# Performance work log

Hardware: AMD Instinct MI355X
Metric: run time of the kernel (lower is better)

## Reference

```python
import jax, jax.numpy as jnp
import numpy as np

M1, M2, BS = 2000, 400, 8
AT = M1 + M2
E1, E2, E3 = 60000, 20000, 20000
H, F, NG, L, C = 64, 64, 50, 4, 4
CUTOFF = 10.0
LOG2 = 0.6931471805599453  # shift of ShiftedSoftplus


def _ssp(x):
    return jax.nn.softplus(x) - LOG2


def _smear(d):
    # GaussianSmearing(0, cutoff, NG)
    offset = jnp.linspace(0.0, CUTOFF, NG)
    coeff = -0.5 / (offset[1] - offset[0]) ** 2
    return jnp.exp(coeff * (d[:, None] - offset[None, :]) ** 2)  # [E, NG]


def _colored_mlp(attr, colors, w1, b1, w2, b2):
    # w1:[C,NG,F] b1:[C,F] w2:[C,F,F] b2:[C,F]; route each edge through its color's MLP
    out = jnp.zeros((attr.shape[0], w1.shape[-1]), attr.dtype)
    for c in range(C):  # fixed small color count
        h = _ssp(attr @ w1[c] + b1[c]) @ w2[c] + b2[c]
        out = out + jnp.where((colors == c)[:, None], h, jnp.zeros((), attr.dtype))
    return out


def _block(h, ei, ew, attr, col, p):
    # InteractionBlock: CFConv -> ssp -> linear
    mw1, mb1, mw2, mb2, cw1, cw2, cb2, bw, bb = p
    Ccut = 0.5 * (jnp.cos(ew * jnp.pi / CUTOFF) + 1.0)
    W = _colored_mlp(attr, col, mw1, mb1, mw2, mb2) * Ccut[:, None]  # [E,F]
    x = h @ cw1                                   # lin1 (no bias) [N,F]
    msg = x[ei[:, 0]] * W                         # gather x_j, modulate
    agg = jax.ops.segment_sum(msg, ei[:, 1], num_segments=h.shape[0])  # scatter-add
    x = agg @ cw2 + cb2                           # lin2
    return _ssp(x) @ bw + bb                      # act + block linear


def _batch_graph(ei, ew, col):
    # replicate per-structure edges across the batch with node offset b*AT
    offs = (jnp.arange(BS, dtype=ei.dtype) * AT)[:, None, None]
    ei_b = (ei[None] + offs).reshape(-1, 2)
    return ei_b, jnp.tile(ew, BS), jnp.tile(col, BS)


def _forward(sites, sites_p, e1, ew1, c1, e2, ew2, c2, e3, ew3, c3,
             emb_w, emb_p_w, mlp_w1, mlp_b1, mlp_w2, mlp_b2,
             conv_w1, conv_w2, conv_b2, blk_w, blk_b,
             out_w1, out_b1, out_w2, out_b2):
    h = jnp.concatenate([emb_w[sites], emb_p_w[sites_p]], axis=1).reshape(BS * AT, H)
    graphs = []
    for (ei, ew, col) in ((e1, ew1, c1), (e2, ew2, c2), (e3, ew3, c3)):
        ei_b, ew_b, col_b = _batch_graph(ei, ew, col)
        graphs.append((ei_b, ew_b, col_b, _smear(ew_b)))
    for l in range(L):
        delta = jnp.zeros_like(h)
        for g, (ei_b, ew_b, col_b, attr_b) in enumerate(graphs):
            p = (mlp_w1[l, g], mlp_b1[l, g], mlp_w2[l, g], mlp_b2[l, g],
                 conv_w1[l, g], conv_w2[l, g], conv_b2[l, g], blk_w[l, g], blk_b[l, g])
            delta = delta + _block(h, ei_b, ew_b, attr_b, col_b, p)
        h = h + delta
    hp = h.reshape(BS, AT, H)[:, M1:, :]   # mask selects pore nodes only
    o = hp @ out_w1 + out_b1               # NB: original has `h - self.act(h)` no-op, so no activation here
    o = o @ out_w2 + out_b2                # [BS, M2, 1]
    return o.sum(axis=1)                   # 'add' readout per batch -> [BS, 1]


def setup_inputs() -> dict:
    key = jax.random.key(0)
    ks = jax.random.split(key, 24)
    f = lambda i, shape, s=0.1: jax.random.normal(ks[i], shape, jnp.float32) * s
    sites = jax.random.randint(ks[0], (BS, M1), 0, 1, dtype=jnp.int32)
    sites_p = jax.random.randint(ks[1], (BS, M2), 0, 2, dtype=jnp.int32)
    e1 = jax.random.randint(ks[2], (E1, 2), 0, M1, dtype=jnp.int32)
    e2 = jnp.stack([jax.random.randint(ks[3], (E2,), 0, M1, dtype=jnp.int32),
                    jax.random.randint(ks[4], (E2,), M1, AT, dtype=jnp.int32)], 1)
    e3 = jnp.stack([jax.random.randint(ks[5], (E3,), M1, AT, dtype=jnp.int32),
                    jax.random.randint(ks[6], (E3,), 0, M1, dtype=jnp.int32)], 1)
    ew1 = jax.random.uniform(ks[7], (E1,), jnp.float32, 0.5, CUTOFF)
    ew2 = jax.random.uniform(ks[8], (E2,), jnp.float32, 0.5, CUTOFF)
    ew3 = jax.random.uniform(ks[9], (E3,), jnp.float32, 0.5, CUTOFF)
    c1 = jax.random.randint(ks[10], (E1,), 0, C, dtype=jnp.int32)
    c2 = jax.random.randint(ks[11], (E2,), 0, C, dtype=jnp.int32)
    c3 = jax.random.randint(ks[12], (E3,), 0, C, dtype=jnp.int32)
    return {
        'sites': sites, 'sites_p': sites_p,
        'edge_idx1': e1, 'edge_weight1': ew1, 'colors1': c1,
        'edge_idx2': e2, 'edge_weight2': ew2, 'colors2': c2,
        'edge_idx3': e3, 'edge_weight3': ew3, 'colors3': c3,
        'emb_w': f(13, (1, H), 1.0), 'emb_p_w': f(14, (2, H), 1.0),
        'mlp_w1': f(15, (L, 3, C, NG, F)), 'mlp_b1': jnp.zeros((L, 3, C, F), jnp.float32),
        'mlp_w2': f(16, (L, 3, C, F, F)), 'mlp_b2': jnp.zeros((L, 3, C, F), jnp.float32),
        'conv_w1': f(17, (L, 3, H, F)), 'conv_w2': f(18, (L, 3, F, H)),
        'conv_b2': jnp.zeros((L, 3, H), jnp.float32),
        'blk_w': f(19, (L, 3, H, H)), 'blk_b': jnp.zeros((L, 3, H), jnp.float32),
        'out_w1': f(20, (H, H // 2)), 'out_b1': jnp.zeros((H // 2,), jnp.float32),
        'out_w2': f(21, (H // 2, 1)), 'out_b2': jnp.zeros((1,), jnp.float32),
    }


def reference(sites, sites_p, edge_idx1, edge_weight1, colors1,
              edge_idx2, edge_weight2, colors2, edge_idx3, edge_weight3, colors3,
              emb_w, emb_p_w, mlp_w1, mlp_b1, mlp_w2, mlp_b2,
              conv_w1, conv_w2, conv_b2, blk_w, blk_b,
              out_w1, out_b1, out_w2, out_b2):
    return _forward(sites, sites_p, edge_idx1, edge_weight1, colors1,
                    edge_idx2, edge_weight2, colors2, edge_idx3, edge_weight3, colors3,
                    emb_w, emb_p_w, mlp_w1, mlp_b1, mlp_w2, mlp_b2,
                    conv_w1, conv_w2, conv_b2, blk_w, blk_b,
                    out_w1, out_b1, out_w2, out_b2)
```

## Files before the change

### kernel.cpp

```cpp
#include <hip/hip_runtime.h>
#include <math.h>

constexpr int M1 = 2000, M2 = 400, BS = 8;
constexpr int AT = M1 + M2;
constexpr int NN = BS * AT;
constexpr int E1 = 60000, E2 = 20000, E3 = 20000;
constexpr int ET = E1 + E2 + E3;
constexpr int H = 64, F = 64, NG = 50, L = 4, C = 4;
constexpr float CUTOFF = 10.0f;
constexpr float LOG2F_ = 0.6931471805599453f;

constexpr float SMEAR_STEP = 10.0f / 49.0f;
constexpr float SMEAR_COEFF = -12.005f;
constexpr float PI_OVER_CUT = 0.31415926535897932f;

constexpr int NBLK = (ET + 255) / 256;

constexpr int NT = 256;
constexpr float DSCALE = (float)(NT - 1) / CUTOFF;

constexpr int GP0 = E1 + 3 * M1;
constexpr int GP1 = E2 + 3 * M2;
constexpr int GP2 = E3 + 3 * M1;
constexpr int ETP = GP0 + GP1 + GP2;

constexpr int TILE_M = 32;

constexpr int SITE_T = M1 / 4;
constexpr int PORE_T = M2 / 4;
constexpr int NBLK_L = 2 * (SITE_T + PORE_T);

constexpr int LT0 = M1 / 4;
constexpr int LT1 = M1 / 4;
constexpr int LT2 = M2 / 4;
constexpr int LTOT = LT0 + LT1 + LT2;
constexpr int PADB = (3 * AT + 255) / 256;

constexpr int A_TAB  = 192;
constexpr int A_INIT = NN * 64 / 256;
constexpr int A_CNT  = NBLK;
constexpr int A_CV   = 3;
constexpr int A_TOT  = A_TAB + A_INIT + A_CNT + A_CV;
constexpr int B_PACK = 48 * NT * 64 / 256;
constexpr int B_TOT  = B_PACK + 3 + 2;

constexpr size_t O_HA    = 0;
constexpr size_t O_HB    = O_HA  + (size_t)NN * 64 * 4;
constexpr size_t O_XG    = O_HB  + (size_t)NN * 64 * 4;
constexpr size_t O_TABF  = O_XG  + (size_t)3 * 2 * AT * 256 * 4;
constexpr size_t O_TAB2  = O_TABF + (size_t)48 * NT * 64 * 4;
constexpr size_t O_EDATA = O_TAB2 + (size_t)48 * NT * 64 * 4;
constexpr size_t O_INT   = O_EDATA + (size_t)ETP * 16;
constexpr int I_DEG  = 0;
constexpr int I_CUR  = 7200;
constexpr int I_ZEND = 14400;
constexpr int I_BASE = 14400;
constexpr int I_PERM = 21616;
constexpr int I_CV   = 26016;

__device__ inline float sspf(float x) {
    return fmaxf(x, 0.0f) + log1pf(expf(-fabsf(x))) - LOG2F_;
}
__device__ inline float sspf_fast(float x) {
    float t = __expf(-fabsf(x));
    return fmaxf(x, 0.0f) + __logf(1.0f + t) - LOG2F_;
}

__device__ inline unsigned int bf16rn(float x) {
    unsigned int u = __float_as_uint(x);
    u = (u + 0x7FFFu + ((u >> 16) & 1u)) >> 16;
    return u & 0xFFFFu;
}

__device__ inline int graph_off(int g) { return g == 0 ? 0 : (g == 1 ? GP0 : GP0 + GP1); }

__device__ inline void edge_decode(int idx, int& g, int& e,
                                   const int* ei1, const int* ei2, const int* ei3,
                                   const int* c1, const int* c2, const int* c3,
                                   const int*& ei, const int*& cl) {
    if (idx < E1)            { g = 0; e = idx;           ei = ei1; cl = c1; }
    else if (idx < E1 + E2)  { g = 1; e = idx - E1;      ei = ei2; cl = c2; }
    else                     { g = 2; e = idx - E1 - E2; ei = ei3; cl = c3; }
}

__global__ __launch_bounds__(256) void k_setupA(
    const float* __restrict__ mlp_w1, const float* __restrict__ mlp_b1,
    const float* __restrict__ mlp_w2, const float* __restrict__ mlp_b2,
    float* __restrict__ tabF,
    const int* __restrict__ sites, const int* __restrict__ sites_p,
    const float* __restrict__ emb_w, const float* __restrict__ emb_p_w,
    float* __restrict__ h,
    const int* __restrict__ ei1, const int* __restrict__ ei2,
    const int* __restrict__ ei3, const int* __restrict__ c1,
    const int* __restrict__ c2, const int* __restrict__ c3,
    int* __restrict__ deg,
    const float* __restrict__ conv_b2, const float* __restrict__ blk_w,
    const float* __restrict__ blk_b, float* __restrict__ cvbuf) {
    int bid = blockIdx.x;
    int t = threadIdx.x;
    if (bid < A_TAB) {
        const int lane = t & 63;
        int wslot = bid * 4 + (t >> 6);
        int s = wslot >> 4;
        int pq = wslot & 15;
        int l = s % L;
        int gc = s / L;
        int c = gc % C;
        int g = gc / C;
        size_t wb = (size_t)((l * 3 + g) * C + c);
        const float* w1 = mlp_w1 + wb * NG * F;
        const float* w2 = mlp_w2 + wb * F * F;
        float w1c[NG], w2c[F];
        #pragma unroll
        for (int k = 0; k < NG; k++) w1c[k] = w1[k * F + lane];
        #pragma unroll
        for (int k = 0; k < F; k++) w2c[k] = w2[k * F + lane];
        float b1c = mlp_b1[wb * F + lane];
        float b2c = mlp_b2[wb * F + lane];
        for (int pp = 0; pp < 16; pp++) {
            int p = pq * 16 + pp;
            float d = (float)p * (CUTOFF / (float)(NT - 1));
            float dd = d - (float)lane * SMEAR_STEP;
            float av = (lane < NG) ? __expf(SMEAR_COEFF * dd * dd) : 0.0f;
            float acc = b1c;
            #pragma unroll
            for (int k = 0; k < NG; k++) acc = fmaf(__shfl(av, k), w1c[k], acc);
            float tt = sspf_fast(acc);
            float acc2 = b2c;
            #pragma unroll
            for (int j = 0; j < F; j++) acc2 = fmaf(__shfl(tt, j), w2c[j], acc2);
            float ccut = 0.5f * (__cosf(d * PI_OVER_CUT) + 1.0f);
            tabF[((size_t)s * NT + p) * 64 + lane] = acc2 * ccut;
        }
    } else if (bid < A_TAB + A_INIT) {
        int idx = (bid - A_TAB) * 256 + t;
        int f = idx & 63;
        int n = idx >> 6;
        int b = n / AT;
        int i = n - b * AT;
        float v;
        if (i < M1) v = emb_w[sites[b * M1 + i] * H + f];
        else        v = emb_p_w[sites_p[b * M2 + (i - M1)] * H + f];
        h[idx] = v;
    } else if (bid < A_TAB + A_INIT + A_CNT) {
        int idx = (bid - A_TAB - A_INIT) * 256 + t;
        if (idx < ET) {
            int g, e; const int* ei; const int* cl;
            edge_decode(idx, g, e, ei1, ei2, ei3, c1, c2, c3, ei, cl);
            atomicAdd(&deg[g * AT + ei[2 * e + 1]], 1);
        }
    } else {
        int s = (bid - A_TAB - A_INIT - A_CNT) * 4 + (t >> 6);
        int lane = t & 63;
        if (s < 12) {
            float sl = sspf(conv_b2[s * 64 + lane]);
            const float* bw = blk_w + (size_t)s * 4096;
            float a = blk_b[s * 64 + lane];
            #pragma unroll 8
            for (int k = 0; k < 64; k++)
                a = fmaf(__shfl(sl, k), bw[k * 64 + lane], a);
            cvbuf[s * 64 + lane] = a;
        }
    }
}

__global__ __launch_bounds__(256) void k_setupB(
    const float* __restrict__ tabF, unsigned int* __restrict__ tab2,
    const int* __restrict__ deg, int* __restrict__ base,
    int* __restrict__ perm) {
    int bid = blockIdx.x;
    int t = threadIdx.x;
    if (bid < B_PACK) {
        int idx = bid * 256 + t;
        int pc = idx & (NT * 64 - 1);
        int nxt = (pc < (NT - 1) * 64) ? idx + 64 : idx;
        unsigned int lo = bf16rn(tabF[idx]);
        unsigned int hi = bf16rn(tabF[nxt]);
        tab2[idx] = lo | (hi << 16);
    } else if (bid < B_PACK + 3) {
        const int T = 256, CH = 10;
        __shared__ int lsum[256];
        int g = bid - B_PACK;
        int loc[CH];
        int s = 0;
        #pragma unroll
        for (int i = 0; i < CH; i++) {
            int idx = t * CH + i;
            int v = (idx < AT) ? ((deg[g * AT + idx] + 3) & ~3) : 0;
            loc[i] = s;
            s += v;
        }
        lsum[t] = s;
        __syncthreads();
        for (int off = 1; off < T; off <<= 1) {
            int v = 0;
            if (t >= off) v = lsum[t - off];
            __syncthreads();
            lsum[t] += v;
            __syncthreads();
        }
        int tb = lsum[t] - s;
        #pragma unroll
        for (int i = 0; i < CH; i++) {
            int idx = t * CH + i;
            if (idx < AT) base[g * (AT + 1) + idx] = tb + loc[i];
        }
        if (t == T - 1) base[g * (AT + 1) + AT] = lsum[T - 1];
    } else {
        __shared__ int hist[256];
        __shared__ int cur[256];
        int q = bid - B_PACK - 3;
        int cnt   = q ? M2 : M1;
        int obase = q ? M1 : 0;
        hist[t] = 0;
        __syncthreads();
        for (int i = t; i < cnt; i += 256) {
            int key = q ? deg[AT + M1 + i] : (deg[i] + deg[2 * AT + i]);
            atomicAdd(&hist[min(key, 255)], 1);
        }
        __syncthreads();
        if (t == 0) {
            int run = 0;
            for (int k = 0; k < 256; k++) { cur[k] = run; run += hist[k]; }
        }
        __syncthreads();
        for (int i = t; i < cnt; i += 256) {
            int key = q ? deg[AT + M1 + i] : (deg[i] + deg[2 * AT + i]);
            int pos = atomicAdd(&cur[min(key, 255)], 1);
            perm[obase + pos] = q ? (M1 + i) : i;
        }
    }
}

__device__ inline void fma4(float acc[4], float a, const float4 b) {
    acc[0] = fmaf(a, b.x, acc[0]);
    acc[1] = fmaf(a, b.y, acc[1]);
    acc[2] = fmaf(a, b.z, acc[2]);
    acc[3] = fmaf(a, b.w, acc[3]);
}

__device__ inline void stage_B(const float* __restrict__ gB, float (*Bs)[68], int t) {
    #pragma unroll
    for (int i = 0; i < 4; i++) {
        int v = t + i * 256;
        int r = v >> 4, c4 = (v & 15) * 4;
        *(float4*)&Bs[r][c4] = *(const float4*)(gB + (size_t)r * 64 + c4);
    }
}
struct WReg { float4 v0, v1, v2, v3; };
__device__ inline WReg stage_ld(const float* __restrict__ g, int t) {
    int r0 = t >> 4, c4 = (t & 15) * 4;
    WReg w;
    w.v0 = *(const float4*)(g + (size_t)r0 * 64 + c4);
    w.v1 = *(const float4*)(g + (size_t)(r0 + 16) * 64 + c4);
    w.v2 = *(const float4*)(g + (size_t)(r0 + 32) * 64 + c4);
    w.v3 = *(const float4*)(g + (size_t)(r0 + 48) * 64 + c4);
    return w;
}
__device__ inline void stage_st(const WReg& w, float (*Bs)[68], int t) {
    int r0 = t >> 4, c4 = (t & 15) * 4;
    *(float4*)&Bs[r0][c4]      = w.v0;
    *(float4*)&Bs[r0 + 16][c4] = w.v1;
    *(float4*)&Bs[r0 + 32][c4] = w.v2;
    *(float4*)&Bs[r0 + 48][c4] = w.v3;
}

__device__ inline void gemm_tile(const float (*As)[68], const float (*Bs)[68],
                                 int r0, int c0, float acc0[4], float acc1[4]) {
    #pragma unroll 4
    for (int k0 = 0; k0 < 64; k0 += 4) {
        float4 a0 = *(const float4*)&As[r0][k0];
        float4 a1 = *(const float4*)&As[r0 + 1][k0];
        float4 b0 = *(const float4*)&Bs[k0][c0];
        float4 b1 = *(const float4*)&Bs[k0 + 1][c0];
        float4 b2 = *(const float4*)&Bs[k0 + 2][c0];
        float4 b3 = *(const float4*)&Bs[k0 + 3][c0];
        fma4(acc0, a0.x, b0); fma4(acc0, a0.y, b1);
        fma4(acc0, a0.z, b2); fma4(acc0, a0.w, b3);
        fma4(acc1, a1.x, b0); fma4(acc1, a1.y, b1);
        fma4(acc1, a1.z, b2); fma4(acc1, a1.w, b3);
    }
}
__device__ inline void gemm_row(const float (*As)[68], const float (*Bs)[68],
                                int r, int c0, float acc[4]) {
    #pragma unroll 4
    for (int k0 = 0; k0 < 64; k0 += 4) {
        float4 a = *(const float4*)&As[r][k0];
        float4 b0 = *(const float4*)&Bs[k0][c0];
        float4 b1 = *(const float4*)&Bs[k0 + 1][c0];
        float4 b2 = *(const float4*)&Bs[k0 + 2][c0];
        float4 b3 = *(const float4*)&Bs[k0 + 3][c0];
        fma4(acc, a.x, b0); fma4(acc, a.y, b1);
        fma4(acc, a.z, b2); fma4(acc, a.w, b3);
    }
}

__device__ inline void xg_store8(const float (*T)[68], float* __restrict__ xg,
                                 int g, int i0, int t) {
    int k = t >> 6, c = t & 63;
    float* o0 = xg + (((size_t)(g * 2 + 0) * AT + i0 + k) * 64 + c) * 4;
    float* o1 = xg + (((size_t)(g * 2 + 1) * AT + i0 + k) * 64 + c) * 4;
    *(float4*)o0 = make_float4(T[k * 8 + 0][c], T[k * 8 + 1][c],
                               T[k * 8 + 2][c], T[k * 8 + 3][c]);
    *(float4*)o1 = make_float4(T[k * 8 + 4][c], T[k * 8 + 5][c],
                               T[k * 8 + 6][c], T[k * 8 + 7][c]);
}
__device__ inline void xg_store4(const float (*T)[68], float* __restrict__ xg,
                                 int g, int bh, const int* __restrict__ perm,
                                 int pbase, int gi, int t) {
    int k = t >> 6, c = t & 63;
    int node = perm[pbase + gi * 4 + k];
    float* out = xg + (((size_t)(g * 2 + bh) * AT + node) * 64 + c) * 4;
    *(float4*)out = make_float4(T[k * 4 + 0][c], T[k * 4 + 1][c],
                                T[k * 4 + 2][c], T[k * 4 + 3][c]);
}

__device__ inline float tab_lerp(unsigned int u, int z) {
    float lo = __uint_as_float(u << 16);
    float hi = __uint_as_float(u & 0xFFFF0000u);
    return fmaf(__int_as_float(z), hi - lo, lo);
}

__device__ inline void gather4(const int4* __restrict__ ed, int s, int e,
                               const unsigned int* __restrict__ tg,
                               const float* __restrict__ xgg,
                               int lane, float acc[4]) {
    for (int i = s; i < e; i += 4) {
        int4 e0 = ed[i];
        int4 e1 = ed[i + 1];
        int4 e2 = ed[i + 2];
        int4 e3 = ed[i + 3];
        unsigned int u0 = tg[(size_t)e0.y * 64 + lane];
        unsigned int u1 = tg[(size_t)e1.y * 64 + lane];
        unsigned int u2 = tg[(size_t)e2.y * 64 + lane];
        unsigned int u3 = tg[(size_t)e3.y * 64 + lane];
        float4 q0 = *(const float4*)(xgg + ((size_t)e0.x << 8) + lane * 4);
        float4 q1 = *(const float4*)(xgg + ((size_t)e1.x << 8) + lane * 4);
        float4 q2 = *(const float4*)(xgg + ((size_t)e2.x << 8) + lane * 4);
        float4 q3 = *(const float4*)(xgg + ((size_t)e3.x << 8) + lane * 4);
        float wl0 = tab_lerp(u0, e0.z);
        float wl1 = tab_lerp(u1, e1.z);
        float wl2 = tab_lerp(u2, e2.z);
        float wl3 = tab_lerp(u3, e3.z);
        fma4(acc, wl0, q0);
        fma4(acc, wl1, q1);
        fma4(acc, wl2, q2);
        fma4(acc, wl3, q3);
    }
}

__global__ __launch_bounds__(256) void k_layer(
    const int4* __restrict__ edata, const int* __restrict__ base,
    const int* __restrict__ perm,
    float* __restrict__ xg, const unsigned int* __restrict__ tab2,
    const float* __restrict__ conv_w2, const float* __restrict__ conv_b2,
    const float* __restrict__ blk_w, const float* __restrict__ blk_b,
    const float* __restrict__ conv_w1, const float* __restrict__ cvbuf,
    const float* __restrict__ hIn, float* __restrict__ hOut,
    int l, int last) {
    __shared__ float As[16][68];
    __shared__ float Ps[16][68];
    __shared__ float Bs[64][68];
    const int t = threadIdx.x;
    const int lane = t & 63;
    const int wv = t >> 6;
    int bid = blockIdx.x;
    int site, tile, bh;
    if (bid < 2 * SITE_T) { site = 1; tile = bid >> 1; bh = bid & 1; }
    else { site = 0; tile = (bid - 2 * SITE_T) >> 1; bh = (bid - 2 * SITE_T) & 1; }
    const int gi = site ? (SITE_T - 1 - tile) : (PORE_T - 1 - tile);
    const int pbperm = site ? 0 : M1;
    const int gA = site ? 0 : 1;
    const size_t pbA = (size_t)(l * 3 + gA);
    const size_t pbB = (size_t)(l * 3 + 2);

    WReg R = stage_ld(conv_w2 + pbA * 4096, t);

    const int dst = __builtin_amdgcn_readfirstlane(perm[pbperm + gi * 4 + wv]);
    float accA[4] = {0, 0, 0, 0}, accB[4] = {0, 0, 0, 0};
    {
        int s = __builtin_amdgcn_readfirstlane(base[gA * (AT + 1) + dst]);
        int e = __builtin_amdgcn_readfirstlane(base[gA * (AT + 1) + dst + 1]);
        gather4(edata + graph_off(gA), s, e,
                tab2 + ((size_t)gA * C * L + l) * NT * 64,
                xg + (size_t)(gA * 2 + bh) * AT * 256, lane, accA);
    }
    if (site) {
        int s = __builtin_amdgcn_readfirstlane(base[2 * (AT + 1) + dst]);
        int e = __builtin_amdgcn_readfirstlane(base[2 * (AT + 1) + dst + 1]);
        gather4(edata + graph_off(2), s, e,
                tab2 + ((size_t)2 * C * L + l) * NT * 64,
                xg + (size_t)(2 * 2 + bh) * AT * 256, lane, accB);
    }
    #pragma unroll
    for (int b = 0; b < 4; b++) As[wv * 4 + b][lane] = accA[b];
    stage_st(R, Bs, t);
    R = stage_ld(blk_w + pbA * 4096, t);
    __syncthreads();

    const int r = t >> 4;
    const int c0 = (t & 15) * 4;
    const int k = r >> 2, bl = r & 3;
    const int node = perm[pbperm + gi * 4 + k];
    const int batch = bh * 4 + bl;
    const size_t o = ((size_t)batch * AT + node) * 64 + c0;
    const float* cvl = cvbuf + (size_t)l * 3 * 64;

    float4 cb = *(const float4*)(conv_b2 + pbA * 64 + c0);
    float x[4] = {cb.x, cb.y, cb.z, cb.w};
    gemm_row(As, Bs, r, c0, x);
    __syncthreads();
    *(float4*)&As[r][c0] =
        make_float4(sspf(x[0]), sspf(x[1]), sspf(x[2]), sspf(x[3]));
    stage_st(R, Bs, t);
    if (site) R = stage_ld(conv_w2 + pbB * 4096, t);
    else if (!last) R = stage_ld(conv_w1 + (size_t)((l + 1) * 3 + 2) * 4096, t);
    __syncthreads();

    float4 hv = *(const float4*)(hIn + o);
    float4 bbA = *(const float4*)(blk_b + pbA * 64 + c0);
    float d[4];
    if (site) {
        float4 bbB = *(const float4*)(blk_b + pbB * 64 + c0);
        float4 cv1 = *(const float4*)(cvl + 64 + c0);
        d[0] = hv.x + bbA.x + bbB.x + cv1.x;
        d[1] = hv.y + bbA.y + bbB.y + cv1.y;
        d[2] = hv.z + bbA.z + bbB.z + cv1.z;
        d[3] = hv.w + bbA.w + bbB.w + cv1.w;
    } else {
        float4 cv0 = *(const float4*)(cvl + c0);
        float4 cv2 = *(const float4*)(cvl + 128 + c0);
        d[0] = hv.x + bbA.x + cv0.x + cv2.x;
        d[1] = hv.y + bbA.y + cv0.y + cv2.y;
        d[2] = hv.z + bbA.z + cv0.z + cv2.z;
        d[3] = hv.w + bbA.w + cv0.w + cv2.w;
    }
    gemm_row(As, Bs, r, c0, d);
    if (site) {
        __syncthreads();
        #pragma unroll
        for (int b = 0; b < 4; b++) As[wv * 4 + b][lane] = accB[b];
        stage_st(R, Bs, t);
        R = stage_ld(blk_w + pbB * 4096, t);
        __syncthreads();
        float4 cb2v = *(const float4*)(conv_b2 + pbB * 64 + c0);
        float y[4] = {cb2v.x, cb2v.y, cb2v.z, cb2v.w};
        gemm_row(As, Bs, r, c0, y);
        __syncthreads();
        *(float4*)&As[r][c0] =
            make_float4(sspf(y[0]), sspf(y[1]), sspf(y[2]), sspf(y[3]));
        stage_st(R, Bs, t);
        if (!last) R = stage_ld(conv_w1 + (size_t)((l + 1) * 3 + 0) * 4096, t);
        __syncthreads();
        gemm_row(As, Bs, r, c0, d);
    }
    *(float4*)(hOut + o) = make_float4(d[0], d[1], d[2], d[3]);
    if (last) return;

    __syncthreads();
    *(float4*)&As[r][c0] = make_float4(d[0], d[1], d[2], d[3]);
    stage_st(R, Bs, t);
    if (site) R = stage_ld(conv_w1 + (size_t)((l + 1) * 3 + 1) * 4096, t);
    __syncthreads();
    float p[4] = {0, 0, 0, 0};
    gemm_row(As, Bs, r, c0, p);
    __syncthreads();
    *(float4*)&Ps[r][c0] = make_float4(p[0], p[1], p[2], p[3]);
    if (site) stage_st(R, Bs, t);
    __syncthreads();
    xg_store4(Ps, xg, site ? 0 : 2, bh, perm, pbperm, gi, t);
    if (site) {
        float q[4] = {0, 0, 0, 0};
        gemm_row(As, Bs, r, c0, q);
        __syncthreads();
        *(float4*)&Ps[r][c0] = make_float4(q[0], q[1], q[2], q[3]);
        __syncthreads();
        xg_store4(Ps, xg, 1, bh, perm, pbperm, gi, t);
    }
}

__global__ __launch_bounds__(256) void k_fl(
    const int* __restrict__ ei1, const int* __restrict__ ei2,
    const int* __restrict__ ei3, const int* __restrict__ c1,
    const int* __restrict__ c2, const int* __restrict__ c3,
    const float* __restrict__ ew1, const float* __restrict__ ew2,
    const float* __restrict__ ew3,
    const int* __restrict__ base, int* __restrict__ cur,
    const int* __restrict__ deg, int4* __restrict__ edata,
    const float* __restrict__ h, const float* __restrict__ conv_w1,
    float* __restrict__ xg) {
    __shared__ float As[TILE_M][68];
    __shared__ float Bs[64][68];
    int t = threadIdx.x;
    if (blockIdx.x >= LTOT + NBLK) {
        int idx = (blockIdx.x - LTOT - NBLK) * 256 + t;
        if (idx >= 3 * AT) return;
        int g = idx / AT, dn = idx - g * AT;
        int d = deg[g * AT + dn];
        int pd = (d + 3) & ~3;
        int4* ep = edata + graph_off(g) + base[g * (AT + 1) + dn] + d;
        for (int k2 = 0; k2 < pd - d; k2++) ep[k2] = make_int4(0, NT - 1, 0, 0);
        return;
    }
    if (blockIdx.x >= LTOT) {
        int idx = (blockIdx.x - LTOT) * 256 + t;
        if (idx >= ET) return;
        int g, e; const int* ei; const int* cl;
        edge_decode(idx, g, e, ei1, ei2, ei3, c1, c2, c3, ei, cl);
        const float* ew = (g == 0) ? ew1 : (g == 1 ? ew2 : ew3);
        int dst = ei[2 * e + 1];
        int src = ei[2 * e];
        int p = base[g * (AT + 1) + dst] + atomicAdd(&cur[g * AT + dst], 1);
        float tt = ew[e] * DSCALE;
        int i0 = min((int)tt, NT - 2);
        float fr = tt - (float)i0;
        int cb = cl[e] * (L * NT) + i0;
        edata[graph_off(g) + p] = make_int4(src, cb, __float_as_int(fr), 0);
        return;
    }
    int g, igrp;
    {
        int bid = blockIdx.x;
        if (bid < LT0)            { g = 0; igrp = bid; }
        else if (bid < LT0 + LT1) { g = 1; igrp = bid - LT0; }
        else                      { g = 2; igrp = LT0 + (bid - LT0 - LT1); }
    }
    int i0 = igrp * 4;
    #pragma unroll
    for (int it = 0; it < 2; it++) {
        int v = t + it * 256;
        int r = v >> 4, c4 = (v & 15) * 4;
        int n = (r & 7) * AT + i0 + (r >> 3);
        *(float4*)&As[r][c4] = *(const float4*)(h + (size_t)n * 64 + c4);
    }
    stage_B(conv_w1 + (size_t)g * 4096, Bs, t);
    __syncthreads();
    int cg = t & 15, rg = t >> 4;
    int c0 = cg * 4, r0 = rg * 2;
    float acc0[4] = {0, 0, 0, 0}, acc1[4] = {0, 0, 0, 0};
    gemm_tile(As, Bs, r0, c0, acc0, acc1);
    __syncthreads();
    *(float4*)&As[r0][c0]     = make_float4(acc0[0], acc0[1], acc0[2], acc0[3]);
    *(float4*)&As[r0 + 1][c0] = make_float4(acc1[0], acc1[1], acc1[2], acc1[3]);
    __syncthreads();
    xg_store8(As, xg, g, i0, t);
}

__global__ void k_read(const float* __restrict__ h,
                       const float* __restrict__ w1, const float* __restrict__ b1,
                       const float* __restrict__ w2, const float* __restrict__ b2,
                       float* __restrict__ out) {
    int b = blockIdx.x;
    int lane = threadIdx.x & 63;
    int wv = threadIdx.x >> 6;
    __shared__ float part[4];
    float weff = 0.0f;
    #pragma unroll
    for (int j = 0; j < H / 2; j++) weff = fmaf(w1[lane * (H / 2) + j], w2[j], weff);
    float acc = 0.0f;
    for (int i = wv * (M2 / 4); i < (wv + 1) * (M2 / 4); i++)
        acc += h[((size_t)b * AT + M1 + i) * H + lane];
    float v = acc * weff;
    for (int off = 32; off; off >>= 1) v += __shfl_xor(v, off);
    if (lane == 0) part[wv] = v;
    __syncthreads();
    if (threadIdx.x == 0) {
        float bias = b2[0];
        for (int j = 0; j < H / 2; j++) bias = fmaf(b1[j], w2[j], bias);
        out[b] = part[0] + part[1] + part[2] + part[3] + (float)M2 * bias;
    }
}

extern "C" void kernel_launch(void* const* d_in, const int* in_sizes, int n_in,
                              void* d_out, int out_size, void* d_ws, size_t ws_size,
                              hipStream_t stream) {
    const int* sites   = (const int*)d_in[0];
    const int* sites_p = (const int*)d_in[1];
    const int* ei1 = (const int*)d_in[2];
    const float* ew1 = (const float*)d_in[3];
    const int* c1 = (const int*)d_in[4];
    const int* ei2 = (const int*)d_in[5];
    const float* ew2 = (const float*)d_in[6];
    const int* c2 = (const int*)d_in[7];
    const int* ei3 = (const int*)d_in[8];
    const float* ew3 = (const float*)d_in[9];
    const int* c3 = (const int*)d_in[10];
    const float* emb_w   = (const float*)d_in[11];
    const float* emb_p_w = (const float*)d_in[12];
    const float* mlp_w1 = (const float*)d_in[13];
    const float* mlp_b1 = (const float*)d_in[14];
    const float* mlp_w2 = (const float*)d_in[15];
    const float* mlp_b2 = (const float*)d_in[16];
    const float* conv_w1 = (const float*)d_in[17];
    const float* conv_w2 = (const float*)d_in[18];
    const float* conv_b2 = (const float*)d_in[19];
    const float* blk_w = (const float*)d_in[20];
    const float* blk_b = (const float*)d_in[21];
    const float* out_w1 = (const float*)d_in[22];
    const float* out_b1 = (const float*)d_in[23];
    const float* out_w2 = (const float*)d_in[24];
    const float* out_b2 = (const float*)d_in[25];

    char* ws = (char*)d_ws;
    float* hA   = (float*)(ws + O_HA);
    float* hB   = (float*)(ws + O_HB);
    float* xg   = (float*)(ws + O_XG);
    float* tabF = (float*)(ws + O_TABF);
    unsigned int* tab2 = (unsigned int*)(ws + O_TAB2);
    int4*  edata = (int4*)(ws + O_EDATA);
    int* ip    = (int*)(ws + O_INT);
    int* deg   = ip + I_DEG;
    int* cur   = ip + I_CUR;
    int* ibase = ip + I_BASE;
    int* dperm = ip + I_PERM;
    float* cvbuf = (float*)(ip + I_CV);

    hipMemsetAsync(ip, 0, (size_t)I_ZEND * sizeof(int), stream);

    k_setupA<<<A_TOT, 256, 0, stream>>>(mlp_w1, mlp_b1, mlp_w2, mlp_b2, tabF,
                                        sites, sites_p, emb_w, emb_p_w, hA,
                                        ei1, ei2, ei3, c1, c2, c3, deg,
                                        conv_b2, blk_w, blk_b, cvbuf);
    k_setupB<<<B_TOT, 256, 0, stream>>>(tabF, tab2, deg, ibase, dperm);
    k_fl<<<LTOT + NBLK + PADB, 256, 0, stream>>>(ei1, ei2, ei3, c1, c2, c3,
                                                 ew1, ew2, ew3, ibase, cur, deg,
                                                 edata, hA, conv_w1, xg);

    float* hcur = hA;
    float* hnxt = hB;
    for (int l = 0; l < L; l++) {
        int last = (l == L - 1) ? 1 : 0;
        k_layer<<<NBLK_L, 256, 0, stream>>>(edata, ibase, dperm, xg, tab2,
                                            conv_w2, conv_b2, blk_w, blk_b,
                                            conv_w1, cvbuf, hcur, hnxt, l, last);
        float* tmp = hcur; hcur = hnxt; hnxt = tmp;
    }
    k_read<<<BS, 256, 0, stream>>>(hcur, out_w1, out_b1, out_w2, out_b2, (float*)d_out);
}
```

Measured before the change: 324.8 us.

## Split fused layer kernel into gather and node kernels with bf16 node features

Replaces the fused per-layer kernel, which gathered messages and then ran the node GEMMs in degree-sorted tiles over half the batch, with two kernels. A gather kernel writes aggregated messages for all 8 batch copies to a global buffer, and a node kernel processes 32-row tiles covering every batch copy. The gathered x features are stored as bf16, packing all 8 batches into one 16-byte load, which halves gather bandwidth and drops the degree-sort permutation. The cost is an extra launch per layer, a round trip of the message buffer through global memory, and lower precision in the gathered features.

```diff
diff --git a/kernel.cpp b/kernel.cpp
--- a/kernel.cpp
+++ b/kernel.cpp
@@ -26,9 +26,11 @@
 
 constexpr int TILE_M = 32;
 
+constexpr int GU  = 4400;
+constexpr int GBLK = GU / 4;
 constexpr int SITE_T = M1 / 4;
 constexpr int PORE_T = M2 / 4;
-constexpr int NBLK_L = 2 * (SITE_T + PORE_T);
+constexpr int NTILE  = SITE_T + PORE_T;
 
 constexpr int LT0 = M1 / 4;
 constexpr int LT1 = M1 / 4;
@@ -42,12 +44,13 @@
 constexpr int A_CV   = 3;
 constexpr int A_TOT  = A_TAB + A_INIT + A_CNT + A_CV;
 constexpr int B_PACK = 48 * NT * 64 / 256;
-constexpr int B_TOT  = B_PACK + 3 + 2;
+constexpr int B_TOT  = B_PACK + 3;
 
 constexpr size_t O_HA    = 0;
 constexpr size_t O_HB    = O_HA  + (size_t)NN * 64 * 4;
 constexpr size_t O_XG    = O_HB  + (size_t)NN * 64 * 4;
-constexpr size_t O_TABF  = O_XG  + (size_t)3 * 2 * AT * 256 * 4;
+constexpr size_t O_MSG   = O_XG  + (size_t)3 * AT * 512 * 2;
+constexpr size_t O_TABF  = O_MSG + (size_t)3 * 8 * AT * 64 * 4;
 constexpr size_t O_TAB2  = O_TABF + (size_t)48 * NT * 64 * 4;
 constexpr size_t O_EDATA = O_TAB2 + (size_t)48 * NT * 64 * 4;
 constexpr size_t O_INT   = O_EDATA + (size_t)ETP * 16;
@@ -55,8 +58,7 @@
 constexpr int I_CUR  = 7200;
 constexpr int I_ZEND = 14400;
 constexpr int I_BASE = 14400;
-constexpr int I_PERM = 21616;
-constexpr int I_CV   = 26016;
+constexpr int I_CV   = 21616;
 
 __device__ inline float sspf(float x) {
     return fmaxf(x, 0.0f) + log1pf(expf(-fabsf(x))) - LOG2F_;
@@ -166,8 +168,7 @@
 
 __global__ __launch_bounds__(256) void k_setupB(
     const float* __restrict__ tabF, unsigned int* __restrict__ tab2,
-    const int* __restrict__ deg, int* __restrict__ base,
-    int* __restrict__ perm) {
+    const int* __restrict__ deg, int* __restrict__ base) {
     int bid = blockIdx.x;
     int t = threadIdx.x;
     if (bid < B_PACK) {
@@ -177,7 +178,7 @@
         unsigned int lo = bf16rn(tabF[idx]);
         unsigned int hi = bf16rn(tabF[nxt]);
         tab2[idx] = lo | (hi << 16);
-    } else if (bid < B_PACK + 3) {
+    } else {
         const int T = 256, CH = 10;
         __shared__ int lsum[256];
         int g = bid - B_PACK;
@@ -206,29 +207,6 @@
             if (idx < AT) base[g * (AT + 1) + idx] = tb + loc[i];
         }
         if (t == T - 1) base[g * (AT + 1) + AT] = lsum[T - 1];
-    } else {
-        __shared__ int hist[256];
-        __shared__ int cur[256];
-        int q = bid - B_PACK - 3;
-        int cnt   = q ? M2 : M1;
-        int obase = q ? M1 : 0;
-        hist[t] = 0;
-        __syncthreads();
-        for (int i = t; i < cnt; i += 256) {
-            int key = q ? deg[AT + M1 + i] : (deg[i] + deg[2 * AT + i]);
-            atomicAdd(&hist[min(key, 255)], 1);
-        }
-        __syncthreads();
-        if (t == 0) {
-            int run = 0;
-            for (int k = 0; k < 256; k++) { cur[k] = run; run += hist[k]; }
-        }
-        __syncthreads();
-        for (int i = t; i < cnt; i += 256) {
-            int key = q ? deg[AT + M1 + i] : (deg[i] + deg[2 * AT + i]);
-            int pos = atomicAdd(&cur[min(key, 255)], 1);
-            perm[obase + pos] = q ? (M1 + i) : i;
-        }
     }
 }
 
@@ -281,38 +259,17 @@
         fma4(acc1, a1.z, b2); fma4(acc1, a1.w, b3);
     }
 }
-__device__ inline void gemm_row(const float (*As)[68], const float (*Bs)[68],
-                                int r, int c0, float acc[4]) {
-    #pragma unroll 4
-    for (int k0 = 0; k0 < 64; k0 += 4) {
-        float4 a = *(const float4*)&As[r][k0];
-        float4 b0 = *(const float4*)&Bs[k0][c0];
-        float4 b1 = *(const float4*)&Bs[k0 + 1][c0];
-        float4 b2 = *(const float4*)&Bs[k0 + 2][c0];
-        float4 b3 = *(const float4*)&Bs[k0 + 3][c0];
-        fma4(acc, a.x, b0); fma4(acc, a.y, b1);
-        fma4(acc, a.z, b2); fma4(acc, a.w, b3);
-    }
-}
-
-__device__ inline void xg_store8(const float (*T)[68], float* __restrict__ xg,
-                                 int g, int i0, int t) {
+
+__device__ inline void xg_transpose_store(const float (*T)[68],
+                                          unsigned short* __restrict__ xg,
+                                          int g, int i0, int t) {
     int k = t >> 6, c = t & 63;
-    float* o0 = xg + (((size_t)(g * 2 + 0) * AT + i0 + k) * 64 + c) * 4;
-    float* o1 = xg + (((size_t)(g * 2 + 1) * AT + i0 + k) * 64 + c) * 4;
-    *(float4*)o0 = make_float4(T[k * 8 + 0][c], T[k * 8 + 1][c],
-                               T[k * 8 + 2][c], T[k * 8 + 3][c]);
-    *(float4*)o1 = make_float4(T[k * 8 + 4][c], T[k * 8 + 5][c],
-                               T[k * 8 + 6][c], T[k * 8 + 7][c]);
-}
-__device__ inline void xg_store4(const float (*T)[68], float* __restrict__ xg,
-                                 int g, int bh, const int* __restrict__ perm,
-                                 int pbase, int gi, int t) {
-    int k = t >> 6, c = t & 63;
-    int node = perm[pbase + gi * 4 + k];
-    float* out = xg + (((size_t)(g * 2 + bh) * AT + node) * 64 + c) * 4;
-    *(float4*)out = make_float4(T[k * 4 + 0][c], T[k * 4 + 1][c],
-                                T[k * 4 + 2][c], T[k * 4 + 3][c]);
+    unsigned int w0 = bf16rn(T[k * 8 + 0][c]) | (bf16rn(T[k * 8 + 1][c]) << 16);
+    unsigned int w1 = bf16rn(T[k * 8 + 2][c]) | (bf16rn(T[k * 8 + 3][c]) << 16);
+    unsigned int w2 = bf16rn(T[k * 8 + 4][c]) | (bf16rn(T[k * 8 + 5][c]) << 16);
+    unsigned int w3 = bf16rn(T[k * 8 + 6][c]) | (bf16rn(T[k * 8 + 7][c]) << 16);
+    unsigned short* out = xg + (((size_t)g * AT + i0 + k) * 64 + c) * 8;
+    *(uint4*)out = make_uint4(w0, w1, w2, w3);
 }
 
 __device__ inline float tab_lerp(unsigned int u, int z) {
@@ -320,11 +277,37 @@
     float hi = __uint_as_float(u & 0xFFFF0000u);
     return fmaf(__int_as_float(z), hi - lo, lo);
 }
-
-__device__ inline void gather4(const int4* __restrict__ ed, int s, int e,
-                               const unsigned int* __restrict__ tg,
-                               const float* __restrict__ xgg,
-                               int lane, float acc[4]) {
+__device__ inline void gmadd8(float acc[8], uint4 q, float wl) {
+    acc[0] = fmaf(__uint_as_float(q.x << 16),         wl, acc[0]);
+    acc[1] = fmaf(__uint_as_float(q.x & 0xFFFF0000u), wl, acc[1]);
+    acc[2] = fmaf(__uint_as_float(q.y << 16),         wl, acc[2]);
+    acc[3] = fmaf(__uint_as_float(q.y & 0xFFFF0000u), wl, acc[3]);
+    acc[4] = fmaf(__uint_as_float(q.z << 16),         wl, acc[4]);
+    acc[5] = fmaf(__uint_as_float(q.z & 0xFFFF0000u), wl, acc[5]);
+    acc[6] = fmaf(__uint_as_float(q.w << 16),         wl, acc[6]);
+    acc[7] = fmaf(__uint_as_float(q.w & 0xFFFF0000u), wl, acc[7]);
+}
+
+__global__ __launch_bounds__(256) void k_gather(
+    const int4* __restrict__ edata, const int* __restrict__ base,
+    const unsigned int* __restrict__ tab2,
+    const unsigned short* __restrict__ xg,
+    float* __restrict__ msg, int l) {
+    const int t = threadIdx.x;
+    const int lane = t & 63;
+    const int u = blockIdx.x * 4 + (t >> 6);
+    int g, dst;
+    if (u < M1)           { g = 0; dst = u; }
+    else if (u < AT)      { g = 1; dst = u; }
+    else                  { g = 2; dst = u - AT; }
+    const int s = base[g * (AT + 1) + dst];
+    const int e = base[g * (AT + 1) + dst + 1];
+    const int4* ed = edata + graph_off(g);
+    const unsigned int* tg = tab2 + ((size_t)g * C * L + l) * NT * 64;
+    const unsigned short* xgg = xg + (size_t)g * AT * 512;
+    float acc[8];
+    #pragma unroll
+    for (int j = 0; j < 8; j++) acc[j] = 0.0f;
     for (int i = s; i < e; i += 4) {
         int4 e0 = ed[i];
         int4 e1 = ed[i + 1];
@@ -334,148 +317,145 @@
         unsigned int u1 = tg[(size_t)e1.y * 64 + lane];
         unsigned int u2 = tg[(size_t)e2.y * 64 + lane];
         unsigned int u3 = tg[(size_t)e3.y * 64 + lane];
-        float4 q0 = *(const float4*)(xgg + ((size_t)e0.x << 8) + lane * 4);
-        float4 q1 = *(const float4*)(xgg + ((size_t)e1.x << 8) + lane * 4);
-        float4 q2 = *(const float4*)(xgg + ((size_t)e2.x << 8) + lane * 4);
-        float4 q3 = *(const float4*)(xgg + ((size_t)e3.x << 8) + lane * 4);
-        float wl0 = tab_lerp(u0, e0.z);
-        float wl1 = tab_lerp(u1, e1.z);
-        float wl2 = tab_lerp(u2, e2.z);
-        float wl3 = tab_lerp(u3, e3.z);
-        fma4(acc, wl0, q0);
-        fma4(acc, wl1, q1);
-        fma4(acc, wl2, q2);
-        fma4(acc, wl3, q3);
-    }
-}
-
-__global__ __launch_bounds__(256) void k_layer(
-    const int4* __restrict__ edata, const int* __restrict__ base,
-    const int* __restrict__ perm,
-    float* __restrict__ xg, const unsigned int* __restrict__ tab2,
+        uint4 q0 = *(const uint4*)(xgg + ((size_t)e0.x * 64 + lane) * 8);
+        uint4 q1 = *(const uint4*)(xgg + ((size_t)e1.x * 64 + lane) * 8);
+        uint4 q2 = *(const uint4*)(xgg + ((size_t)e2.x * 64 + lane) * 8);
+        uint4 q3 = *(const uint4*)(xgg + ((size_t)e3.x * 64 + lane) * 8);
+        gmadd8(acc, q0, tab_lerp(u0, e0.z));
+        gmadd8(acc, q1, tab_lerp(u1, e1.z));
+        gmadd8(acc, q2, tab_lerp(u2, e2.z));
+        gmadd8(acc, q3, tab_lerp(u3, e3.z));
+    }
+    float* mp = msg + ((size_t)g * 8 * AT + dst) * 64 + lane;
+    #pragma unroll
+    for (int b = 0; b < 8; b++) mp[(size_t)b * AT * 64] = acc[b];
+}
+
+__global__ __launch_bounds__(256) void k_node(
+    const float* __restrict__ msg,
     const float* __restrict__ conv_w2, const float* __restrict__ conv_b2,
     const float* __restrict__ blk_w, const float* __restrict__ blk_b,
     const float* __restrict__ conv_w1, const float* __restrict__ cvbuf,
     const float* __restrict__ hIn, float* __restrict__ hOut,
-    int l, int last) {
-    __shared__ float As[16][68];
-    __shared__ float Ps[16][68];
+    unsigned short* __restrict__ xg, int l, int last) {
+    __shared__ float As[TILE_M][68];
+    __shared__ float Ps[TILE_M][68];
     __shared__ float Bs[64][68];
     const int t = threadIdx.x;
-    const int lane = t & 63;
-    const int wv = t >> 6;
-    int bid = blockIdx.x;
-    int site, tile, bh;
-    if (bid < 2 * SITE_T) { site = 1; tile = bid >> 1; bh = bid & 1; }
-    else { site = 0; tile = (bid - 2 * SITE_T) >> 1; bh = (bid - 2 * SITE_T) & 1; }
-    const int gi = site ? (SITE_T - 1 - tile) : (PORE_T - 1 - tile);
-    const int pbperm = site ? 0 : M1;
+    const int bid = blockIdx.x;
+    const int site = (bid < SITE_T) ? 1 : 0;
+    const int i0 = site ? bid * 4 : M1 + (bid - SITE_T) * 4;
     const int gA = site ? 0 : 1;
     const size_t pbA = (size_t)(l * 3 + gA);
     const size_t pbB = (size_t)(l * 3 + 2);
 
     WReg R = stage_ld(conv_w2 + pbA * 4096, t);
-
-    const int dst = __builtin_amdgcn_readfirstlane(perm[pbperm + gi * 4 + wv]);
-    float accA[4] = {0, 0, 0, 0}, accB[4] = {0, 0, 0, 0};
-    {
-        int s = __builtin_amdgcn_readfirstlane(base[gA * (AT + 1) + dst]);
-        int e = __builtin_amdgcn_readfirstlane(base[gA * (AT + 1) + dst + 1]);
-        gather4(edata + graph_off(gA), s, e,
-                tab2 + ((size_t)gA * C * L + l) * NT * 64,
-                xg + (size_t)(gA * 2 + bh) * AT * 256, lane, accA);
-    }
-    if (site) {
-        int s = __builtin_amdgcn_readfirstlane(base[2 * (AT + 1) + dst]);
-        int e = __builtin_amdgcn_readfirstlane(base[2 * (AT + 1) + dst + 1]);
-        gather4(edata + graph_off(2), s, e,
-                tab2 + ((size_t)2 * C * L + l) * NT * 64,
-                xg + (size_t)(2 * 2 + bh) * AT * 256, lane, accB);
-    }
     #pragma unroll
-    for (int b = 0; b < 4; b++) As[wv * 4 + b][lane] = accA[b];
+    for (int it = 0; it < 2; it++) {
+        int v = t + it * 256;
+        int r = v >> 4, c4 = (v & 15) * 4;
+        int k = r >> 3, b = r & 7;
+        *(float4*)&As[r][c4] =
+            *(const float4*)(msg + (((size_t)gA * 8 + b) * AT + i0 + k) * 64 + c4);
+    }
     stage_st(R, Bs, t);
     R = stage_ld(blk_w + pbA * 4096, t);
     __syncthreads();
 
-    const int r = t >> 4;
-    const int c0 = (t & 15) * 4;
-    const int k = r >> 2, bl = r & 3;
-    const int node = perm[pbperm + gi * 4 + k];
-    const int batch = bh * 4 + bl;
-    const size_t o = ((size_t)batch * AT + node) * 64 + c0;
+    const int cg = t & 15, rg = t >> 4;
+    const int c0 = cg * 4, r0 = rg * 2;
     const float* cvl = cvbuf + (size_t)l * 3 * 64;
 
     float4 cb = *(const float4*)(conv_b2 + pbA * 64 + c0);
-    float x[4] = {cb.x, cb.y, cb.z, cb.w};
-    gemm_row(As, Bs, r, c0, x);
-    __syncthreads();
-    *(float4*)&As[r][c0] =
-        make_float4(sspf(x[0]), sspf(x[1]), sspf(x[2]), sspf(x[3]));
+    float x0[4] = {cb.x, cb.y, cb.z, cb.w};
+    float x1[4] = {cb.x, cb.y, cb.z, cb.w};
+    gemm_tile(As, Bs, r0, c0, x0, x1);
+    __syncthreads();
+    *(float4*)&As[r0][c0] =
+        make_float4(sspf(x0[0]), sspf(x0[1]), sspf(x0[2]), sspf(x0[3]));
+    *(float4*)&As[r0 + 1][c0] =
+        make_float4(sspf(x1[0]), sspf(x1[1]), sspf(x1[2]), sspf(x1[3]));
     stage_st(R, Bs, t);
     if (site) R = stage_ld(conv_w2 + pbB * 4096, t);
     else if (!last) R = stage_ld(conv_w1 + (size_t)((l + 1) * 3 + 2) * 4096, t);
     __syncthreads();
 
-    float4 hv = *(const float4*)(hIn + o);
+    const int k0r = r0 >> 3, b0r = r0 & 7;
+    const size_t o0 = ((size_t)b0r * AT + i0 + k0r) * 64 + c0;
+    const int k1r = (r0 + 1) >> 3, b1r = (r0 + 1) & 7;
+    const size_t o1 = ((size_t)b1r * AT + i0 + k1r) * 64 + c0;
+    float4 h0 = *(const float4*)(hIn + o0);
+    float4 h1 = *(const float4*)(hIn + o1);
     float4 bbA = *(const float4*)(blk_b + pbA * 64 + c0);
-    float d[4];
+    float4 ex;
     if (site) {
         float4 bbB = *(const float4*)(blk_b + pbB * 64 + c0);
         float4 cv1 = *(const float4*)(cvl + 64 + c0);
-        d[0] = hv.x + bbA.x + bbB.x + cv1.x;
-        d[1] = hv.y + bbA.y + bbB.y + cv1.y;
-        d[2] = hv.z + bbA.z + bbB.z + cv1.z;
-        d[3] = hv.w + bbA.w + bbB.w + cv1.w;
+        ex = make_float4(bbB.x + cv1.x, bbB.y + cv1.y, bbB.z + cv1.z, bbB.w + cv1.w);
     } else {
         float4 cv0 = *(const float4*)(cvl + c0);
         float4 cv2 = *(const float4*)(cvl + 128 + c0);
-        d[0] = hv.x + bbA.x + cv0.x + cv2.x;
-        d[1] = hv.y + bbA.y + cv0.y + cv2.y;
-        d[2] = hv.z + bbA.z + cv0.z + cv2.z;
-        d[3] = hv.w + bbA.w + cv0.w + cv2.w;
-    }
-    gemm_row(As, Bs, r, c0, d);
+        ex = make_float4(cv0.x + cv2.x, cv0.y + cv2.y, cv0.z + cv2.z, cv0.w + cv2.w);
+    }
+    float d0[4] = {h0.x + bbA.x + ex.x, h0.y + bbA.y + ex.y,
+                   h0.z + bbA.z + ex.z, h0.w + bbA.w + ex.w};
+    float d1[4] = {h1.x + bbA.x + ex.x, h1.y + bbA.y + ex.y,
+                   h1.z + bbA.z + ex.z, h1.w + bbA.w + ex.w};
+    gemm_tile(As, Bs, r0, c0, d0, d1);
+
     if (site) {
         __syncthreads();
         #pragma unroll
-        for (int b = 0; b < 4; b++) As[wv * 4 + b][lane] = accB[b];
+        for (int it = 0; it < 2; it++) {
+            int v = t + it * 256;
+            int r = v >> 4, c4 = (v & 15) * 4;
+            int k = r >> 3, b = r & 7;
+            *(float4*)&As[r][c4] =
+                *(const float4*)(msg + (((size_t)2 * 8 + b) * AT + i0 + k) * 64 + c4);
+        }
         stage_st(R, Bs, t);
         R = stage_ld(blk_w + pbB * 4096, t);
         __syncthreads();
         float4 cb2v = *(const float4*)(conv_b2 + pbB * 64 + c0);
-        float y[4] = {cb2v.x, cb2v.y, cb2v.z, cb2v.w};
-        gemm_row(As, Bs, r, c0, y);
+        float y0[4] = {cb2v.x, cb2v.y, cb2v.z, cb2v.w};
+        float y1[4] = {cb2v.x, cb2v.y, cb2v.z, cb2v.w};
+        gemm_tile(As, Bs, r0, c0, y0, y1);
         __syncthreads();
-        *(float4*)&As[r][c0] =
-            make_float4(sspf(y[0]), sspf(y[1]), sspf(y[2]), sspf(y[3]));
+        *(float4*)&As[r0][c0] =
+            make_float4(sspf(y0[0]), sspf(y0[1]), sspf(y0[2]), sspf(y0[3]));
+        *(float4*)&As[r0 + 1][c0] =
+            make_float4(sspf(y1[0]), sspf(y1[1]), sspf(y1[2]), sspf(y1[3]));
         stage_st(R, Bs, t);
         if (!last) R = stage_ld(conv_w1 + (size_t)((l + 1) * 3 + 0) * 4096, t);
         __syncthreads();
-        gemm_row(As, Bs, r, c0, d);
-    }
-    *(float4*)(hOut + o) = make_float4(d[0], d[1], d[2], d[3]);
+        gemm_tile(As, Bs, r0, c0, d0, d1);
+    }
+    *(float4*)(hOut + o0) = make_float4(d0[0], d0[1], d0[2], d0[3]);
+    *(float4*)(hOut + o1) = make_float4(d1[0], d1[1], d1[2], d1[3]);
     if (last) return;
 
     __syncthreads();
-    *(float4*)&As[r][c0] = make_float4(d[0], d[1], d[2], d[3]);
+    *(float4*)&As[r0][c0]     = make_float4(d0[0], d0[1], d0[2], d0[3]);
+    *(float4*)&As[r0 + 1][c0] = make_float4(d1[0], d1[1], d1[2], d1[3]);
     stage_st(R, Bs, t);
     if (site) R = stage_ld(conv_w1 + (size_t)((l + 1) * 3 + 1) * 4096, t);
     __syncthreads();
-    float p[4] = {0, 0, 0, 0};
-    gemm_row(As, Bs, r, c0, p);
-    __syncthreads();
-    *(float4*)&Ps[r][c0] = make_float4(p[0], p[1], p[2], p[3]);
+    float p0[4] = {0, 0, 0, 0}, p1[4] = {0, 0, 0, 0};
+    gemm_tile(As, Bs, r0, c0, p0, p1);
+    __syncthreads();
+    *(float4*)&Ps[r0][c0]     = make_float4(p0[0], p0[1], p0[2], p0[3]);
+    *(float4*)&Ps[r0 + 1][c0] = make_float4(p1[0], p1[1], p1[2], p1[3]);
     if (site) stage_st(R, Bs, t);
     __syncthreads();
-    xg_store4(Ps, xg, site ? 0 : 2, bh, perm, pbperm, gi, t);
+    xg_transpose_store(Ps, xg, site ? 0 : 2, i0, t);
     if (site) {
-        float q[4] = {0, 0, 0, 0};
-        gemm_row(As, Bs, r, c0, q);
+        float q0[4] = {0, 0, 0, 0}, q1[4] = {0, 0, 0, 0};
+        gemm_tile(As, Bs, r0, c0, q0, q1);
         __syncthreads();
-        *(float4*)&Ps[r][c0] = make_float4(q[0], q[1], q[2], q[3]);
+        *(float4*)&Ps[r0][c0]     = make_float4(q0[0], q0[1], q0[2], q0[3]);
+        *(float4*)&Ps[r0 + 1][c0] = make_float4(q1[0], q1[1], q1[2], q1[3]);
         __syncthreads();
-        xg_store4(Ps, xg, 1, bh, perm, pbperm, gi, t);
+        xg_transpose_store(Ps, xg, 1, i0, t);
     }
 }
 
@@ -488,7 +468,7 @@
     const int* __restrict__ base, int* __restrict__ cur,
     const int* __restrict__ deg, int4* __restrict__ edata,
     const float* __restrict__ h, const float* __restrict__ conv_w1,
-    float* __restrict__ xg) {
+    unsigned short* __restrict__ xg) {
     __shared__ float As[TILE_M][68];
     __shared__ float Bs[64][68];
     int t = threadIdx.x;
@@ -543,7 +523,7 @@
     *(float4*)&As[r0][c0]     = make_float4(acc0[0], acc0[1], acc0[2], acc0[3]);
     *(float4*)&As[r0 + 1][c0] = make_float4(acc1[0], acc1[1], acc1[2], acc1[3]);
     __syncthreads();
-    xg_store8(As, xg, g, i0, t);
+    xg_transpose_store(As, xg, g, i0, t);
 }
 
 __global__ void k_read(const float* __restrict__ h,
@@ -604,7 +584,8 @@
     char* ws = (char*)d_ws;
     float* hA   = (float*)(ws + O_HA);
     float* hB   = (float*)(ws + O_HB);
-    float* xg   = (float*)(ws + O_XG);
+    unsigned short* xg = (unsigned short*)(ws + O_XG);
+    float* msg  = (float*)(ws + O_MSG);
     float* tabF = (float*)(ws + O_TABF);
     unsigned int* tab2 = (unsigned int*)(ws + O_TAB2);
     int4*  edata = (int4*)(ws + O_EDATA);
@@ -612,7 +593,6 @@
     int* deg   = ip + I_DEG;
     int* cur   = ip + I_CUR;
     int* ibase = ip + I_BASE;
-    int* dperm = ip + I_PERM;
     float* cvbuf = (float*)(ip + I_CV);
 
     hipMemsetAsync(ip, 0, (size_t)I_ZEND * sizeof(int), stream);
@@ -621,7 +601,7 @@
                                         sites, sites_p, emb_w, emb_p_w, hA,
                                         ei1, ei2, ei3, c1, c2, c3, deg,
                                         conv_b2, blk_w, blk_b, cvbuf);
-    k_setupB<<<B_TOT, 256, 0, stream>>>(tabF, tab2, deg, ibase, dperm);
+    k_setupB<<<B_TOT, 256, 0, stream>>>(tabF, tab2, deg, ibase);
     k_fl<<<LTOT + NBLK + PADB, 256, 0, stream>>>(ei1, ei2, ei3, c1, c2, c3,
                                                  ew1, ew2, ew3, ibase, cur, deg,
                                                  edata, hA, conv_w1, xg);
@@ -630,9 +610,9 @@
     float* hnxt = hB;
     for (int l = 0; l < L; l++) {
         int last = (l == L - 1) ? 1 : 0;
-        k_layer<<<NBLK_L, 256, 0, stream>>>(edata, ibase, dperm, xg, tab2,
-                                            conv_w2, conv_b2, blk_w, blk_b,
-                                            conv_w1, cvbuf, hcur, hnxt, l, last);
+        k_gather<<<GBLK, 256, 0, stream>>>(edata, ibase, tab2, xg, msg, l);
+        k_node<<<NTILE, 256, 0, stream>>>(msg, conv_w2, conv_b2, blk_w, blk_b,
+                                          conv_w1, cvbuf, hcur, hnxt, xg, l, last);
         float* tmp = hcur; hcur = hnxt; hnxt = tmp;
     }
     k_read<<<BS, 256, 0, stream>>>(hcur, out_w1, out_b1, out_w2, out_b2, (float*)d_out);
```

New measurement: 327.1 us. About the same (+0.7%).
